# Optimization experiments

Hardware: AMD Instinct MI355X
Metric: run time of the kernel (lower is better)

## Reference

```python
import jax, jax.numpy as jnp
import numpy as np

GROUP_SIZE = 128
IN_FEATURES = 8192
OUT_FEATURES = 28672
TOKENS = 32


def _dequantize(qweight, qzeros, scales):
    """ExLlama q4 dequant.
    qweight: (K//8, N) int32, 8 int4 values per word packed along k.
    qzeros:  (G, N//8) int32, 8 int4 zeros per word packed along n.
    scales:  (G, N) fp16.  g = k // GROUP_SIZE; w = s * (q - (z + 1)).
    """
    shifts = jnp.arange(8, dtype=jnp.int32) * 4
    K = qweight.shape[0] * 8
    N = qweight.shape[1]
    G = qzeros.shape[0]
    # unpack weights along k: (K//8, 8, N) -> (K, N)
    q = (qweight[:, None, :] >> shifts[None, :, None]) & 15
    q = q.reshape(K, N)
    # unpack zeros along n: (G, N//8, 8) -> (G, N)
    z = (qzeros[:, :, None] >> shifts[None, None, :]) & 15
    z = z.reshape(G, N)
    # group-wise dequant: reshape k into (G, GROUP_SIZE)
    qg = q.reshape(G, GROUP_SIZE, N).astype(jnp.float16)
    zf = (z + 1).astype(jnp.float16)[:, None, :]          # ExLlama stores zero-1
    w = (qg - zf) * scales[:, None, :]                    # (G, GS, N) fp16
    return w.reshape(K, N)


def setup_inputs() -> dict:
    key = jax.random.key(0)
    k1, k2, k3, k4, k5 = jax.random.split(key, 5)
    x = jax.random.normal(k1, (TOKENS, IN_FEATURES), dtype=jnp.float16)
    qweight = jax.random.randint(k2, (IN_FEATURES // 8, OUT_FEATURES),
                                 minval=-(2**31), maxval=2**31 - 1, dtype=jnp.int32)
    qzeros = jax.random.randint(k3, (IN_FEATURES // GROUP_SIZE, OUT_FEATURES // 8),
                                minval=-(2**31), maxval=2**31 - 1, dtype=jnp.int32)
    scales = (jax.random.uniform(k4, (IN_FEATURES // GROUP_SIZE, OUT_FEATURES),
                                 dtype=jnp.float32) * 0.01 + 0.001).astype(jnp.float16)
    bias = jax.random.normal(k5, (OUT_FEATURES,), dtype=jnp.float16)
    return {"x": x, "qweight": qweight, "qzeros": qzeros,
            "scales": scales, "bias": bias}


def reference(x, qweight, qzeros, scales, bias):
    w = _dequantize(qweight, qzeros, scales)              # (K, N) fp16
    out = jnp.matmul(x.astype(jnp.float16), w)            # (T, N)
    return out + bias
```

## Files before the change

### kernel.cpp

```cpp
#include <hip/hip_runtime.h>

#define T_TOK   32
#define KDIM    8192
#define NDIM    28672
#define NZW     3584
#define NSEG    16
#define SEGK    (KDIM / NSEG)
#define GPS     4

typedef _Float16 half8  __attribute__((ext_vector_type(8)));
typedef _Float16 half2v __attribute__((ext_vector_type(2)));
typedef float    f32x4  __attribute__((ext_vector_type(4)));
typedef unsigned uint4v __attribute__((ext_vector_type(4)));

typedef const __attribute__((address_space(1))) void gas_void;
typedef __attribute__((address_space(3))) void       las_void;

__global__ __launch_bounds__(256)
void xprep(const float* __restrict__ x, _Float16* __restrict__ xp)
{
    const int idx = blockIdx.x * 256 + threadIdx.x;
    const int t   = idx >> 10;
    const int k0  = (idx & 1023) * 8;
    const float* src = x + (size_t)t * KDIM + k0;
    f32x4 lo = *(const f32x4*)src;
    f32x4 hi = *(const f32x4*)(src + 4);
    uint4v u;
    #pragma unroll
    for (int j = 0; j < 4; ++j)
        u[j] = __builtin_bit_cast(unsigned,
                  __builtin_amdgcn_cvt_pkrtz(lo[j], hi[j]));
    *(uint4v*)(xp + (size_t)t * KDIM + k0) = u;
}

__global__ __launch_bounds__(256)
void exllama_gemm_glds(const int*      __restrict__ qweight,
                       const int*      __restrict__ qzeros,
                       const float*    __restrict__ scales,
                       const _Float16* __restrict__ xp,
                       _Float16*       __restrict__ ws)
{
    __shared__ alignas(16) _Float16 xs[T_TOK * SEGK];
    char* xb = (char*)xs;

    const int tid  = threadIdx.x;
    const int lane = tid & 63;
    const int wav  = tid >> 6;
    const int quad = lane >> 4;
    const int l16  = lane & 15;
    const int seg  = blockIdx.y;
    const int n0   = blockIdx.x * 128 + wav * 32;
    const int g0   = seg * GPS;
    const int kseg0 = seg * SEGK;

    int nc[2];
    nc[0] = n0 + l16;
    nc[1] = n0 + 16 + l16;

    unsigned qw[GPS][8];
    #pragma unroll
    for (int g = 0; g < GPS; ++g) {
        const size_t rb = (size_t)((g0 + g) * 16 + quad) * NDIM;
        #pragma unroll
        for (int c = 0; c < 4; ++c)
            #pragma unroll
            for (int j = 0; j < 2; ++j)
                qw[g][c * 2 + j] = (unsigned)qweight[rb + (size_t)(c * 4) * NDIM + nc[j]];
    }

    float sraw[GPS][2];
    int   zraw[GPS][2];
    #pragma unroll
    for (int g = 0; g < GPS; ++g)
        #pragma unroll
        for (int j = 0; j < 2; ++j) {
            sraw[g][j] = scales[(size_t)(g0 + g) * NDIM + nc[j]];
            zraw[g][j] = qzeros[(size_t)(g0 + g) * NZW + (nc[j] >> 3)];
        }

    __builtin_amdgcn_sched_barrier(0);

    {
        #pragma unroll
        for (int it = 0; it < 8; ++it) {
            const int c = it * 256 + tid;
            const int v = c ^ ((c >> 6) & 7);
            const int t = c >> 6;
            const _Float16* src = xp + (size_t)t * KDIM + kseg0 + (v & 63) * 8;
            __builtin_amdgcn_global_load_lds(
                (gas_void*)src,
                (las_void*)(xb + it * 4096 + wav * 1024),
                16, 0, 0);
        }
    }

    half2v sp[GPS][2], cp[GPS][2];
    #pragma unroll
    for (int g = 0; g < GPS; ++g)
        #pragma unroll
        for (int j = 0; j < 2; ++j) {
            const int z = (zraw[g][j] >> ((nc[j] & 7) * 4)) & 15;
            const _Float16 sh = (_Float16)sraw[g][j];
            const _Float16 ch = (_Float16)(float)(-(1025 + z));
            sp[g][j] = (half2v){sh, sh};
            cp[g][j] = (half2v){ch, ch};
        }

    __syncthreads();

    f32x4 acc[2][2];
    #pragma unroll
    for (int j = 0; j < 2; ++j)
        #pragma unroll
        for (int m = 0; m < 2; ++m)
            acc[j][m] = (f32x4){0.f, 0.f, 0.f, 0.f};

    #pragma unroll
    for (int g = 0; g < GPS; ++g) {
        #pragma unroll
        for (int c = 0; c < 4; ++c) {
            const int kloc = g * 128 + c * 32 + quad * 8;
            const int o0 = (l16 * 1024 + kloc * 2) ^ ((l16 & 7) << 4);
            half8 a0 = *(const half8*)(xb + o0);
            half8 a1 = *(const half8*)(xb + o0 + 16 * 1024);
            #pragma unroll
            for (int j = 0; j < 2; ++j) {
                const unsigned w = qw[g][c * 2 + j];
                uint4v bu;
                #pragma unroll
                for (int i = 0; i < 4; ++i) {
                    unsigned t = ((w >> (4 * i)) & 0x000F000Fu) | 0x64006400u;
                    half2v th = __builtin_bit_cast(half2v, t);
                    half2v r  = (th + cp[g][j]) * sp[g][j];
                    bu[i] = __builtin_bit_cast(unsigned, r);
                }
                half8 bf = __builtin_bit_cast(half8, bu);
                acc[j][0] = __builtin_amdgcn_mfma_f32_16x16x32_f16(a0, bf, acc[j][0], 0, 0, 0);
                acc[j][1] = __builtin_amdgcn_mfma_f32_16x16x32_f16(a1, bf, acc[j][1], 0, 0, 0);
            }
        }
    }

    _Float16* wsp = ws + (size_t)seg * (T_TOK * NDIM);
    #pragma unroll
    for (int j = 0; j < 2; ++j)
        #pragma unroll
        for (int m = 0; m < 2; ++m)
            #pragma unroll
            for (int r = 0; r < 4; ++r) {
                const int t = m * 16 + quad * 4 + r;
                wsp[(size_t)t * NDIM + nc[j]] = (_Float16)acc[j][m][r];
            }
}

__global__ __launch_bounds__(256)
void reduce_bias(const _Float16* __restrict__ ws,
                 const float*    __restrict__ bias,
                 float*          __restrict__ out)
{
    const int e = (blockIdx.x * 256 + threadIdx.x) * 8;
    const int n = e % NDIM;
    float sum[8] = {0.f, 0.f, 0.f, 0.f, 0.f, 0.f, 0.f, 0.f};
    #pragma unroll
    for (int s = 0; s < NSEG; ++s) {
        half8 v = *(const half8*)(ws + (size_t)s * (T_TOK * NDIM) + e);
        #pragma unroll
        for (int i = 0; i < 8; ++i) sum[i] += (float)v[i];
    }
    f32x4 o0, o1;
    #pragma unroll
    for (int i = 0; i < 4; ++i) {
        o0[i] = sum[i]     + bias[n + i];
        o1[i] = sum[i + 4] + bias[n + 4 + i];
    }
    *(f32x4*)(out + e)     = o0;
    *(f32x4*)(out + e + 4) = o1;
}

__global__ __launch_bounds__(256)
void exllama_gemm_atomic(const int*   __restrict__ qweight,
                         const int*   __restrict__ qzeros,
                         const float* __restrict__ scales,
                         const float* __restrict__ x,
                         const float* __restrict__ bias,
                         float*       __restrict__ out)
{
    __shared__ alignas(16) _Float16 xs[T_TOK * SEGK];
    char* xb = (char*)xs;

    const int tid  = threadIdx.x;
    const int lane = tid & 63;
    const int wav  = tid >> 6;
    const int quad = lane >> 4;
    const int l16  = lane & 15;
    const int seg  = blockIdx.y;
    const int n0   = blockIdx.x * 128 + wav * 32;
    const int g0   = seg * GPS;

    int nc[2];
    nc[0] = n0 + l16;
    nc[1] = n0 + 16 + l16;

    unsigned qw[GPS][8];
    #pragma unroll
    for (int g = 0; g < GPS; ++g) {
        const size_t rb = (size_t)((g0 + g) * 16 + quad) * NDIM;
        #pragma unroll
        for (int c = 0; c < 4; ++c)
            #pragma unroll
            for (int j = 0; j < 2; ++j)
                qw[g][c * 2 + j] = (unsigned)qweight[rb + (size_t)(c * 4) * NDIM + nc[j]];
    }
    float sraw[GPS][2];
    int   zraw[GPS][2];
    #pragma unroll
    for (int g = 0; g < GPS; ++g)
        #pragma unroll
        for (int j = 0; j < 2; ++j) {
            sraw[g][j] = scales[(size_t)(g0 + g) * NDIM + nc[j]];
            zraw[g][j] = qzeros[(size_t)(g0 + g) * NZW + (nc[j] >> 3)];
        }
    {
        const int kseg0 = seg * SEGK;
        #pragma unroll
        for (int it = 0; it < 8; ++it) {
            const int e  = it * 2048 + tid * 8;
            const int t  = e >> 9;
            const int kl = e & (SEGK - 1);
            const float* xpr = x + (size_t)t * KDIM + kseg0 + kl;
            f32x4 lo = *(const f32x4*)xpr;
            f32x4 hi = *(const f32x4*)(xpr + 4);
            uint4v u;
            #pragma unroll
            for (int j = 0; j < 4; ++j)
                u[j] = __builtin_bit_cast(unsigned,
                          __builtin_amdgcn_cvt_pkrtz(lo[j], hi[j]));
            const int off = (t * 1024 + kl * 2) ^ ((t & 7) << 4);
            *(uint4v*)(xb + off) = u;
        }
    }
    half2v sp[GPS][2], cp[GPS][2];
    #pragma unroll
    for (int g = 0; g < GPS; ++g)
        #pragma unroll
        for (int j = 0; j < 2; ++j) {
            const int z = (zraw[g][j] >> ((nc[j] & 7) * 4)) & 15;
            const _Float16 sh = (_Float16)sraw[g][j];
            const _Float16 ch = (_Float16)(float)(-(1025 + z));
            sp[g][j] = (half2v){sh, sh};
            cp[g][j] = (half2v){ch, ch};
        }
    __syncthreads();

    f32x4 acc[2][2];
    #pragma unroll
    for (int j = 0; j < 2; ++j)
        #pragma unroll
        for (int m = 0; m < 2; ++m)
            acc[j][m] = (f32x4){0.f, 0.f, 0.f, 0.f};
    #pragma unroll
    for (int g = 0; g < GPS; ++g) {
        #pragma unroll
        for (int c = 0; c < 4; ++c) {
            const int kloc = g * 128 + c * 32 + quad * 8;
            const int o0 = (l16 * 1024 + kloc * 2) ^ ((l16 & 7) << 4);
            half8 a0 = *(const half8*)(xb + o0);
            half8 a1 = *(const half8*)(xb + o0 + 16 * 1024);
            #pragma unroll
            for (int j = 0; j < 2; ++j) {
                const unsigned w = qw[g][c * 2 + j];
                uint4v bu;
                #pragma unroll
                for (int i = 0; i < 4; ++i) {
                    unsigned t = ((w >> (4 * i)) & 0x000F000Fu) | 0x64006400u;
                    half2v th = __builtin_bit_cast(half2v, t);
                    half2v r  = (th + cp[g][j]) * sp[g][j];
                    bu[i] = __builtin_bit_cast(unsigned, r);
                }
                half8 bf = __builtin_bit_cast(half8, bu);
                acc[j][0] = __builtin_amdgcn_mfma_f32_16x16x32_f16(a0, bf, acc[j][0], 0, 0, 0);
                acc[j][1] = __builtin_amdgcn_mfma_f32_16x16x32_f16(a1, bf, acc[j][1], 0, 0, 0);
            }
        }
    }
    #pragma unroll
    for (int j = 0; j < 2; ++j) {
        const float bb = bias[nc[j]] * (1.0f / NSEG);
        #pragma unroll
        for (int m = 0; m < 2; ++m)
            #pragma unroll
            for (int r = 0; r < 4; ++r) {
                const int t = m * 16 + quad * 4 + r;
                unsafeAtomicAdd(out + (size_t)t * NDIM + nc[j], acc[j][m][r] + bb);
            }
    }
}

extern "C" void kernel_launch(void* const* d_in, const int* in_sizes, int n_in,
                              void* d_out, int out_size, void* d_ws, size_t ws_size,
                              hipStream_t stream)
{
    const float* x  = (const float*)d_in[0];
    const int* qweight = (const int*)d_in[1];
    const int* qzeros  = (const int*)d_in[2];
    const float* sc = (const float*)d_in[3];
    const float* bs = (const float*)d_in[4];
    float* out      = (float*)d_out;

    const size_t xpbytes = (size_t)T_TOK * KDIM * sizeof(_Float16);
    const size_t pbytes  = (size_t)NSEG * T_TOK * NDIM * sizeof(_Float16);
    if (ws_size >= xpbytes + pbytes) {
        _Float16* xp   = (_Float16*)d_ws;
        _Float16* part = xp + (size_t)T_TOK * KDIM;
        xprep<<<(T_TOK * KDIM / 8) / 256, 256, 0, stream>>>(x, xp);
        exllama_gemm_glds<<<dim3(NDIM / 128, NSEG), 256, 0, stream>>>(
            qweight, qzeros, sc, xp, part);
        reduce_bias<<<(T_TOK * NDIM) / (256 * 8), 256, 0, stream>>>(
            part, bs, out);
    } else {
        exllama_gemm_atomic<<<dim3(NDIM / 128, NSEG), 256, 0, stream>>>(
            qweight, qzeros, sc, x, bs, out);
    }
}
```

Before: 199.2 us.

## Stage qweight tile into LDS via wide async global_load_lds with swizzle

The main GEMM kernel now copies the block's full qweight tile (64 rows by 128 columns) into LDS with 16-byte global_load_lds transfers, replacing per-thread 4-byte scattered global loads held in registers. Each wave then reads its packed words from LDS using an XOR swizzle meant to avoid bank conflicts. The aim is wider, better-coalesced weight fetches and fewer live registers. In exchange, LDS use doubles to 64KB per block, which can lower occupancy, and the weights take an extra LDS round trip before dequantisation.

```diff
diff --git a/kernel.cpp b/kernel.cpp
--- a/kernel.cpp
+++ b/kernel.cpp
@@ -7,6 +7,7 @@
 #define NSEG    16
 #define SEGK    (KDIM / NSEG)
 #define GPS     4
+#define QROWS   (SEGK / 8)
 
 typedef _Float16 half8  __attribute__((ext_vector_type(8)));
 typedef _Float16 half2v __attribute__((ext_vector_type(2)));
@@ -34,11 +35,164 @@
 }
 
 __global__ __launch_bounds__(256)
-void exllama_gemm_glds(const int*      __restrict__ qweight,
+void exllama_gemm_wide(const int*      __restrict__ qweight,
                        const int*      __restrict__ qzeros,
                        const float*    __restrict__ scales,
                        const _Float16* __restrict__ xp,
                        _Float16*       __restrict__ ws)
+{
+    __shared__ alignas(16) char smem[65536];
+    char* xb  = smem;
+    char* qwb = smem + 32768;
+
+    const int tid  = threadIdx.x;
+    const int lane = tid & 63;
+    const int wav  = tid >> 6;
+    const int quad = lane >> 4;
+    const int l16  = lane & 15;
+    const int seg  = blockIdx.y;
+    const int nblk = blockIdx.x * 128;
+    const int n0   = nblk + wav * 32;
+    const int g0   = seg * GPS;
+    const int kseg0 = seg * SEGK;
+    const int qrow0 = seg * QROWS;
+
+    int nc[2];
+    nc[0] = n0 + l16;
+    nc[1] = n0 + 16 + l16;
+
+    #pragma unroll
+    for (int it = 0; it < 8; ++it) {
+        const int c    = it * 256 + tid;
+        const int r    = c >> 5;
+        const int dcol = (c & 31) * 4;
+        const int scol = dcol ^ ((r & 3) << 3);
+        const int* src = qweight + (size_t)(qrow0 + r) * NDIM + nblk + scol;
+        __builtin_amdgcn_global_load_lds(
+            (gas_void*)src,
+            (las_void*)(qwb + it * 4096 + wav * 1024),
+            16, 0, 0);
+    }
+
+    #pragma unroll
+    for (int it = 0; it < 8; ++it) {
+        const int c = it * 256 + tid;
+        const int v = c ^ ((c >> 6) & 7);
+        const int t = c >> 6;
+        const _Float16* src = xp + (size_t)t * KDIM + kseg0 + (v & 63) * 8;
+        __builtin_amdgcn_global_load_lds(
+            (gas_void*)src,
+            (las_void*)(xb + it * 4096 + wav * 1024),
+            16, 0, 0);
+    }
+
+    float sraw[GPS][2];
+    int   zraw[GPS][2];
+    #pragma unroll
+    for (int g = 0; g < GPS; ++g)
+        #pragma unroll
+        for (int j = 0; j < 2; ++j) {
+            sraw[g][j] = scales[(size_t)(g0 + g) * NDIM + nc[j]];
+            zraw[g][j] = qzeros[(size_t)(g0 + g) * NZW + (nc[j] >> 3)];
+        }
+
+    half2v sp[GPS][2], cp[GPS][2];
+    #pragma unroll
+    for (int g = 0; g < GPS; ++g)
+        #pragma unroll
+        for (int j = 0; j < 2; ++j) {
+            const int z = (zraw[g][j] >> ((nc[j] & 7) * 4)) & 15;
+            const _Float16 sh = (_Float16)sraw[g][j];
+            const _Float16 ch = (_Float16)(float)(-(1025 + z));
+            sp[g][j] = (half2v){sh, sh};
+            cp[g][j] = (half2v){ch, ch};
+        }
+
+    __syncthreads();
+
+    f32x4 acc[2][2];
+    #pragma unroll
+    for (int j = 0; j < 2; ++j)
+        #pragma unroll
+        for (int m = 0; m < 2; ++m)
+            acc[j][m] = (f32x4){0.f, 0.f, 0.f, 0.f};
+
+    const int cb0 = wav * 32 + l16;
+    const int cb1 = cb0 + 16;
+    const int swz = quad << 3;
+
+    #pragma unroll
+    for (int g = 0; g < GPS; ++g) {
+        #pragma unroll
+        for (int c = 0; c < 4; ++c) {
+            const int kloc = g * 128 + c * 32 + quad * 8;
+            const int o0 = (l16 * 1024 + kloc * 2) ^ ((l16 & 7) << 4);
+            half8 a0 = *(const half8*)(xb + o0);
+            half8 a1 = *(const half8*)(xb + o0 + 16 * 1024);
+            const int row = g * 16 + c * 4 + quad;
+            const unsigned w0 = *(const unsigned*)(qwb + row * 512 + ((cb0 ^ swz) * 4));
+            const unsigned w1 = *(const unsigned*)(qwb + row * 512 + ((cb1 ^ swz) * 4));
+            #pragma unroll
+            for (int j = 0; j < 2; ++j) {
+                const unsigned w = j ? w1 : w0;
+                uint4v bu;
+                #pragma unroll
+                for (int i = 0; i < 4; ++i) {
+                    unsigned t = ((w >> (4 * i)) & 0x000F000Fu) | 0x64006400u;
+                    half2v th = __builtin_bit_cast(half2v, t);
+                    half2v r  = (th + cp[g][j]) * sp[g][j];
+                    bu[i] = __builtin_bit_cast(unsigned, r);
+                }
+                half8 bf = __builtin_bit_cast(half8, bu);
+                acc[j][0] = __builtin_amdgcn_mfma_f32_16x16x32_f16(a0, bf, acc[j][0], 0, 0, 0);
+                acc[j][1] = __builtin_amdgcn_mfma_f32_16x16x32_f16(a1, bf, acc[j][1], 0, 0, 0);
+            }
+        }
+    }
+
+    _Float16* wsp = ws + (size_t)seg * (T_TOK * NDIM);
+    #pragma unroll
+    for (int j = 0; j < 2; ++j)
+        #pragma unroll
+        for (int m = 0; m < 2; ++m)
+            #pragma unroll
+            for (int r = 0; r < 4; ++r) {
+                const int t = m * 16 + quad * 4 + r;
+                wsp[(size_t)t * NDIM + nc[j]] = (_Float16)acc[j][m][r];
+            }
+}
+
+__global__ __launch_bounds__(256)
+void reduce_bias(const _Float16* __restrict__ ws,
+                 const float*    __restrict__ bias,
+                 float*          __restrict__ out)
+{
+    const int e = (blockIdx.x * 256 + threadIdx.x) * 8;
+    const int n = e % NDIM;
+    float sum[8] = {0.f, 0.f, 0.f, 0.f, 0.f, 0.f, 0.f, 0.f};
+    #pragma unroll
+    for (int s = 0; s < NSEG; ++s) {
+        half8 v = *(const half8*)(ws + (size_t)s * (T_TOK * NDIM) + e);
+        #pragma unroll
+        for (int i = 0; i < 8; ++i) sum[i] += (float)v[i];
+    }
+    f32x4 o0, o1;
+    #pragma unroll
+    for (int i = 0; i < 4; ++i) {
+        o0[i] = sum[i]     + bias[n + i];
+        o1[i] = sum[i + 4] + bias[n + 4 + i];
+    }
+    *(f32x4*)(out + e)     = o0;
+    *(f32x4*)(out + e + 4) = o1;
+}
+
+__global__ __launch_bounds__(256)
+void exllama_gemm_atomic(const int*   __restrict__ qweight,
+                         const int*   __restrict__ qzeros,
+                         const float* __restrict__ scales,
+                         const float* __restrict__ x,
+                         const float* __restrict__ bias,
+                         float*       __restrict__ out)
 {
     __shared__ alignas(16) _Float16 xs[T_TOK * SEGK];
     char* xb = (char*)xs;
@@ -51,7 +205,6 @@
     const int seg  = blockIdx.y;
     const int n0   = blockIdx.x * 128 + wav * 32;
     const int g0   = seg * GPS;
-    const int kseg0 = seg * SEGK;
 
     int nc[2];
     nc[0] = n0 + l16;
@@ -67,7 +220,6 @@
             for (int j = 0; j < 2; ++j)
                 qw[g][c * 2 + j] = (unsigned)qweight[rb + (size_t)(c * 4) * NDIM + nc[j]];
     }
-
     float sraw[GPS][2];
     int   zraw[GPS][2];
     #pragma unroll
@@ -77,23 +229,25 @@
             sraw[g][j] = scales[(size_t)(g0 + g) * NDIM + nc[j]];
             zraw[g][j] = qzeros[(size_t)(g0 + g) * NZW + (nc[j] >> 3)];
         }
-
-    __builtin_amdgcn_sched_barrier(0);
-
     {
+        const int kseg0 = seg * SEGK;
         #pragma unroll
         for (int it = 0; it < 8; ++it) {
-            const int c = it * 256 + tid;
-            const int v = c ^ ((c >> 6) & 7);
-            const int t = c >> 6;
-            const _Float16* src = xp + (size_t)t * KDIM + kseg0 + (v & 63) * 8;
-            __builtin_amdgcn_global_load_lds(
-                (gas_void*)src,
-                (las_void*)(xb + it * 4096 + wav * 1024),
-                16, 0, 0);
-        }
-    }
-
+            const int e  = it * 2048 + tid * 8;
+            const int t  = e >> 9;
+            const int kl = e & (SEGK - 1);
+            const float* xpr = x + (size_t)t * KDIM + kseg0 + kl;
+            f32x4 lo = *(const f32x4*)xpr;
+            f32x4 hi = *(const f32x4*)(xpr + 4);
+            uint4v u;
+            #pragma unroll
+            for (int j = 0; j < 4; ++j)
+                u[j] = __builtin_bit_cast(unsigned,
+                          __builtin_amdgcn_cvt_pkrtz(lo[j], hi[j]));
+            const int off = (t * 1024 + kl * 2) ^ ((t & 7) << 4);
+            *(uint4v*)(xb + off) = u;
+        }
+    }
     half2v sp[GPS][2], cp[GPS][2];
     #pragma unroll
     for (int g = 0; g < GPS; ++g)
@@ -105,7 +259,6 @@
             sp[g][j] = (half2v){sh, sh};
             cp[g][j] = (half2v){ch, ch};
         }
-
     __syncthreads();
 
     f32x4 acc[2][2];
@@ -114,7 +267,6 @@
         #pragma unroll
         for (int m = 0; m < 2; ++m)
             acc[j][m] = (f32x4){0.f, 0.f, 0.f, 0.f};
-
     #pragma unroll
     for (int g = 0; g < GPS; ++g) {
         #pragma unroll
@@ -140,149 +292,6 @@
             }
         }
     }
-
-    _Float16* wsp = ws + (size_t)seg * (T_TOK * NDIM);
-    #pragma unroll
-    for (int j = 0; j < 2; ++j)
-        #pragma unroll
-        for (int m = 0; m < 2; ++m)
-            #pragma unroll
-            for (int r = 0; r < 4; ++r) {
-                const int t = m * 16 + quad * 4 + r;
-                wsp[(size_t)t * NDIM + nc[j]] = (_Float16)acc[j][m][r];
-            }
-}
-
-__global__ __launch_bounds__(256)
-void reduce_bias(const _Float16* __restrict__ ws,
-                 const float*    __restrict__ bias,
-                 float*          __restrict__ out)
-{
-    const int e = (blockIdx.x * 256 + threadIdx.x) * 8;
-    const int n = e % NDIM;
-    float sum[8] = {0.f, 0.f, 0.f, 0.f, 0.f, 0.f, 0.f, 0.f};
-    #pragma unroll
-    for (int s = 0; s < NSEG; ++s) {
-        half8 v = *(const half8*)(ws + (size_t)s * (T_TOK * NDIM) + e);
-        #pragma unroll
-        for (int i = 0; i < 8; ++i) sum[i] += (float)v[i];
-    }
-    f32x4 o0, o1;
-    #pragma unroll
-    for (int i = 0; i < 4; ++i) {
-        o0[i] = sum[i]     + bias[n + i];
-        o1[i] = sum[i + 4] + bias[n + 4 + i];
-    }
-    *(f32x4*)(out + e)     = o0;
-    *(f32x4*)(out + e + 4) = o1;
-}
-
-__global__ __launch_bounds__(256)
-void exllama_gemm_atomic(const int*   __restrict__ qweight,
-                         const int*   __restrict__ qzeros,
-                         const float* __restrict__ scales,
-                         const float* __restrict__ x,
-                         const float* __restrict__ bias,
-                         float*       __restrict__ out)
-{
-    __shared__ alignas(16) _Float16 xs[T_TOK * SEGK];
-    char* xb = (char*)xs;
-
-    const int tid  = threadIdx.x;
-    const int lane = tid & 63;
-    const int wav  = tid >> 6;
-    const int quad = lane >> 4;
-    const int l16  = lane & 15;
-    const int seg  = blockIdx.y;
-    const int n0   = blockIdx.x * 128 + wav * 32;
-    const int g0   = seg * GPS;
-
-    int nc[2];
-    nc[0] = n0 + l16;
-    nc[1] = n0 + 16 + l16;
-
-    unsigned qw[GPS][8];
-    #pragma unroll
-    for (int g = 0; g < GPS; ++g) {
-        const size_t rb = (size_t)((g0 + g) * 16 + quad) * NDIM;
-        #pragma unroll
-        for (int c = 0; c < 4; ++c)
-            #pragma unroll
-            for (int j = 0; j < 2; ++j)
-                qw[g][c * 2 + j] = (unsigned)qweight[rb + (size_t)(c * 4) * NDIM + nc[j]];
-    }
-    float sraw[GPS][2];
-    int   zraw[GPS][2];
-    #pragma unroll
-    for (int g = 0; g < GPS; ++g)
-        #pragma unroll
-        for (int j = 0; j < 2; ++j) {
-            sraw[g][j] = scales[(size_t)(g0 + g) * NDIM + nc[j]];
-            zraw[g][j] = qzeros[(size_t)(g0 + g) * NZW + (nc[j] >> 3)];
-        }
-    {
-        const int kseg0 = seg * SEGK;
-        #pragma unroll
-        for (int it = 0; it < 8; ++it) {
-            const int e  = it * 2048 + tid * 8;
-            const int t  = e >> 9;
-            const int kl = e & (SEGK - 1);
-            const float* xpr = x + (size_t)t * KDIM + kseg0 + kl;
-            f32x4 lo = *(const f32x4*)xpr;
-            f32x4 hi = *(const f32x4*)(xpr + 4);
-            uint4v u;
-            #pragma unroll
-            for (int j = 0; j < 4; ++j)
-                u[j] = __builtin_bit_cast(unsigned,
-                          __builtin_amdgcn_cvt_pkrtz(lo[j], hi[j]));
-            const int off = (t * 1024 + kl * 2) ^ ((t & 7) << 4);
-            *(uint4v*)(xb + off) = u;
-        }
-    }
-    half2v sp[GPS][2], cp[GPS][2];
-    #pragma unroll
-    for (int g = 0; g < GPS; ++g)
-        #pragma unroll
-        for (int j = 0; j < 2; ++j) {
-            const int z = (zraw[g][j] >> ((nc[j] & 7) * 4)) & 15;
-            const _Float16 sh = (_Float16)sraw[g][j];
-            const _Float16 ch = (_Float16)(float)(-(1025 + z));
-            sp[g][j] = (half2v){sh, sh};
-            cp[g][j] = (half2v){ch, ch};
-        }
-    __syncthreads();
-
-    f32x4 acc[2][2];
-    #pragma unroll
-    for (int j = 0; j < 2; ++j)
-        #pragma unroll
-        for (int m = 0; m < 2; ++m)
-            acc[j][m] = (f32x4){0.f, 0.f, 0.f, 0.f};
-    #pragma unroll
-    for (int g = 0; g < GPS; ++g) {
-        #pragma unroll
-        for (int c = 0; c < 4; ++c) {
-            const int kloc = g * 128 + c * 32 + quad * 8;
-            const int o0 = (l16 * 1024 + kloc * 2) ^ ((l16 & 7) << 4);
-            half8 a0 = *(const half8*)(xb + o0);
-            half8 a1 = *(const half8*)(xb + o0 + 16 * 1024);
-            #pragma unroll
-            for (int j = 0; j < 2; ++j) {
-                const unsigned w = qw[g][c * 2 + j];
-                uint4v bu;
-                #pragma unroll
-                for (int i = 0; i < 4; ++i) {
-                    unsigned t = ((w >> (4 * i)) & 0x000F000Fu) | 0x64006400u;
-                    half2v th = __builtin_bit_cast(half2v, t);
-                    half2v r  = (th + cp[g][j]) * sp[g][j];
-                    bu[i] = __builtin_bit_cast(unsigned, r);
-                }
-                half8 bf = __builtin_bit_cast(half8, bu);
-                acc[j][0] = __builtin_amdgcn_mfma_f32_16x16x32_f16(a0, bf, acc[j][0], 0, 0, 0);
-                acc[j][1] = __builtin_amdgcn_mfma_f32_16x16x32_f16(a1, bf, acc[j][1], 0, 0, 0);
-            }
-        }
-    }
     #pragma unroll
     for (int j = 0; j < 2; ++j) {
         const float bb = bias[nc[j]] * (1.0f / NSEG);
@@ -313,7 +322,7 @@
         _Float16* xp   = (_Float16*)d_ws;
         _Float16* part = xp + (size_t)T_TOK * KDIM;
         xprep<<<(T_TOK * KDIM / 8) / 256, 256, 0, stream>>>(x, xp);
-        exllama_gemm_glds<<<dim3(NDIM / 128, NSEG), 256, 0, stream>>>(
+        exllama_gemm_wide<<<dim3(NDIM / 128, NSEG), 256, 0, stream>>>(
             qweight, qzeros, sc, xp, part);
         reduce_bias<<<(T_TOK * NDIM) / (256 * 8), 256, 0, stream>>>(
             part, bs, out);
```

New measurement: 199.8 us. About the same (+0.3%).
